# Kernel tuning notes

Hardware: AMD Instinct MI355X
Metric: run time of the kernel (lower is better)

Reference implementation:

```python
import jax, jax.numpy as jnp
import numpy as np
import math

B, CK, CV, O, T, H, W = 2, 64, 512, 2, 16, 30, 54


def setup_inputs() -> dict:
    key = jax.random.key(0)
    k1, k2, k3, k4, k5 = jax.random.split(key, 5)
    return {
        'query_key': jax.random.normal(k1, (B, CK, H, W), jnp.float32),
        'query_selection': jax.random.uniform(k2, (B, CK, H, W), jnp.float32),
        'memory_key': jax.random.normal(k3, (B, CK, T, H, W), jnp.float32),
        'memory_shrinkage': jax.random.uniform(k4, (B, 1, T, H, W), jnp.float32),
        'memory_value': jax.random.normal(k5, (B, O, CV, T, H, W), jnp.float32),
    }


def reference(query_key, query_selection, memory_key, memory_shrinkage, memory_value):
    b, ck, h, w = query_key.shape
    t = memory_key.shape[2]
    n = t * h * w          # memory bank size
    hw = h * w             # query size
    o, cv = memory_value.shape[1], memory_value.shape[2]

    mk = memory_key.reshape(b, ck, n)             # B CK N
    ms = memory_shrinkage.reshape(b, 1, n)        # B 1 N
    qk = query_key.reshape(b, ck, hw)             # B CK HW
    qe = query_selection.reshape(b, ck, hw)       # B CK HW

    # negative squared L2 distance, selection-weighted per channel:
    # -sum_c qe_c * (mk_c - qk_c)^2 = -a_sq + 2ab - b_sq
    a_sq = jnp.einsum('bcn,bcq->bnq', mk * mk, qe)          # B N HW
    two_ab = 2.0 * jnp.einsum('bcn,bcq->bnq', mk, qk * qe)  # B N HW
    b_sq = jnp.sum(qe * qk * qk, axis=1, keepdims=True)     # B 1 HW
    similarity = (-a_sq + two_ab - b_sq)
    # shrinkage scaling + 1/sqrt(CK)
    similarity = similarity * ms.reshape(b, n, 1) * (1.0 / math.sqrt(ck))

    # softmax over the memory axis N
    affinity = jax.nn.softmax(similarity, axis=1)           # B N HW

    # weighted readout
    mv = memory_value.reshape(b, o * cv, n)                 # B (O*CV) N
    mem = jnp.einsum('bvn,bnq->bvq', mv, affinity)          # B (O*CV) HW
    return mem.reshape(b, o, cv, h, w)
```

## Files before the change

kernel.cpp:

```cpp
#include <hip/hip_runtime.h>
#include <stdint.h>

#define CKP 128
#define OCV 1024
#define NTOT 25920
#define HW 1620
#define HWP 1664
#define QT 128
#define VT 256
#define NC 64
#define NQT 13
#define NVT 4
#define CHUNKS_TOTAL 405

typedef _Float16 f16x8 __attribute__((ext_vector_type(8)));
typedef _Float16 f16x4 __attribute__((ext_vector_type(4)));
typedef float f32x4 __attribute__((ext_vector_type(4)));

__device__ __forceinline__ void gload_lds16(const void* g, void* l) {
  __builtin_amdgcn_global_load_lds(
      (const __attribute__((address_space(1))) uint32_t*)g,
      (__attribute__((address_space(3))) uint32_t*)l, 16, 0, 0);
}

__global__ void k_prep_mv(const float* __restrict__ mv, _Float16* __restrict__ mvh) {
  int i = blockIdx.x * 256 + threadIdx.x;
  const float4* s = (const float4*)mv + (size_t)i * 2;
  float4 a = s[0], b = s[1];
  f16x8 o;
  o[0]=(_Float16)a.x; o[1]=(_Float16)a.y; o[2]=(_Float16)a.z; o[3]=(_Float16)a.w;
  o[4]=(_Float16)b.x; o[5]=(_Float16)b.y; o[6]=(_Float16)b.z; o[7]=(_Float16)b.w;
  *((f16x8*)mvh + i) = o;
}

__global__ void k_prep_mk(const float* __restrict__ mk, _Float16* __restrict__ mkp) {
  __shared__ _Float16 LT[64 * CKP];
  int b = blockIdx.y, n0 = blockIdx.x * 64;
  int c4 = threadIdx.x >> 6, nl = threadIdx.x & 63;
  for (int c = c4; c < 64; c += 4) {
    float v = mk[((size_t)(b * 64 + c)) * NTOT + n0 + nl];
    LT[nl * CKP + c]      = (_Float16)v;
    LT[nl * CKP + 64 + c] = (_Float16)(v * v);
  }
  __syncthreads();
  #pragma unroll
  for (int k = 0; k < 4; ++k) {
    int idx = threadIdx.x + 256 * k;
    int n = idx >> 4, c16 = idx & 15;
    *((uint4*)(mkp + ((size_t)b * NTOT + n0 + n) * CKP + c16 * 8)) =
        *((const uint4*)(&LT[n * CKP + c16 * 8]));
  }
}

__global__ void k_prep_q(const float* __restrict__ qk, const float* __restrict__ qe,
                         _Float16* __restrict__ qp, float* __restrict__ bsq) {
  __shared__ _Float16 LT[QT * CKP];
  int b = blockIdx.y, q0 = blockIdx.x * QT;
  int t = threadIdx.x;
  int q = q0 + t;
  bool valid = q < HW;
  float acc = 0.f;
  for (int c = 0; c < 64; ++c) {
    float a = valid ? qk[((size_t)(b * 64 + c)) * HW + q] : 0.f;
    float e = valid ? qe[((size_t)(b * 64 + c)) * HW + q] : 0.f;
    LT[t * CKP + c]      = (_Float16)(2.f * a * e);
    LT[t * CKP + 64 + c] = (_Float16)(-e);
    acc += e * a * a;
  }
  bsq[(size_t)b * HWP + q] = acc;
  __syncthreads();
  #pragma unroll
  for (int k = 0; k < 16; ++k) {
    int idx = t + 128 * k;
    int qq = idx >> 4, c16 = idx & 15;
    *((uint4*)(qp + ((size_t)b * HWP + q0 + qq) * CKP + c16 * 8)) =
        *((const uint4*)(&LT[qq * CKP + c16 * 8]));
  }
}

__launch_bounds__(512, 1)
__global__ void k_main(const _Float16* __restrict__ mvh, const _Float16* __restrict__ mkp,
                       const _Float16* __restrict__ qp, const float* __restrict__ bsq,
                       const float* __restrict__ ms,
                       float* __restrict__ pO, float* __restrict__ lpart,
                       int NS, int CPN) {
  const int qt = blockIdx.x, vt = blockIdx.y;
  const int b = blockIdx.z & 1, nsp = blockIdx.z >> 1;
  const int tid = threadIdx.x;
  const int w = tid >> 6, l = tid & 63;
  const int l15 = l & 15, g = l >> 4;

  __shared__ _Float16 MVs[2][VT * NC];
  __shared__ _Float16 MKs[2][NC * CKP];
  __shared__ _Float16 Ps[2][QT * NC];
  __shared__ float lred[QT * 8];

  const int qw = w & 3, nh = w >> 2;
  const int wv = w & 3, wq = w >> 2;

  const int cBeg = nsp * CPN;
  int ce = cBeg + CPN; if (ce > CHUNKS_TOTAL) ce = CHUNKS_TOTAL;
  const int cEnd = ce;

  const char* mvb[4]; int dmv[4];
  #pragma unroll
  for (int k = 0; k < 4; ++k) {
    int idx = k * 512 + tid;
    int v = idx >> 3, s = idx & 7, j = s ^ (v & 7);
    mvb[k] = (const char*)(mvh + ((size_t)b * OCV + vt * VT + v) * NTOT + j * 8);
    dmv[k] = idx * 16;
  }
  const char* mkb[2]; int dmk[2];
  #pragma unroll
  for (int k = 0; k < 2; ++k) {
    int idx = k * 512 + tid;
    int n = idx >> 4, s = idx & 15, j = s ^ (n & 7);
    mkb[k] = (const char*)(mkp + ((size_t)b * NTOT + n) * CKP + j * 8);
    dmk[k] = idx * 16;
  }
  const float* msb = ms + (size_t)b * NTOT + nh * 32 + g * 4;

  f16x8 qreg[2][4];
  float bq[2];
  #pragma unroll
  for (int j = 0; j < 2; ++j) {
    int q_loc = qw * 32 + j * 16 + l15;
    const _Float16* qrow = qp + ((size_t)b * HWP + qt * QT + q_loc) * CKP;
    #pragma unroll
    for (int ks = 0; ks < 4; ++ks) qreg[j][ks] = *((const f16x8*)(qrow + (ks * 4 + g) * 8));
    bq[j] = bsq[(size_t)b * HWP + qt * QT + q_loc];
  }

  f32x4 acc[4][4];
  #pragma unroll
  for (int i = 0; i < 4; ++i)
    #pragma unroll
    for (int j = 0; j < 4; ++j) acc[i][j] = (f32x4)0.f;
  float lp0 = 0.f, lp1 = 0.f;

  auto stage_mv = [&](int ch, int buf) {
    size_t o = (size_t)ch * (NC * 2);
    char* d = (char*)MVs[buf];
    #pragma unroll
    for (int k = 0; k < 4; ++k) gload_lds16(mvb[k] + o, d + dmv[k]);
  };
  auto stage_mk = [&](int ch, int buf) {
    size_t o = (size_t)ch * (NC * CKP * 2);
    char* d = (char*)MKs[buf];
    #pragma unroll
    for (int k = 0; k < 2; ++k) gload_lds16(mkb[k] + o, d + dmk[k]);
  };

  auto do_S = [&](int kb, int pb, float4 mA, float4 mB) {
    const _Float16* MKc = MKs[kb];
    f32x4 sacc[2][2];
    #pragma unroll
    for (int i2 = 0; i2 < 2; ++i2)
      #pragma unroll
      for (int j = 0; j < 2; ++j) sacc[i2][j] = (f32x4)0.f;
    #pragma unroll
    for (int ks = 0; ks < 4; ++ks) {
      f16x8 af[2];
      #pragma unroll
      for (int i2 = 0; i2 < 2; ++i2) {
        int n_loc = nh * 32 + i2 * 16 + l15;
        af[i2] = *((const f16x8*)(&MKc[n_loc * CKP + (((ks * 4 + g) ^ (n_loc & 7)) * 8)]));
      }
      #pragma unroll
      for (int i2 = 0; i2 < 2; ++i2)
        #pragma unroll
        for (int j = 0; j < 2; ++j)
          sacc[i2][j] = __builtin_amdgcn_mfma_f32_16x16x32_f16(af[i2], qreg[j][ks], sacc[i2][j], 0, 0, 0);
    }
    const float K = 0.125f * 1.44269504f;
    #pragma unroll
    for (int i2 = 0; i2 < 2; ++i2) {
      int nbase = nh * 32 + i2 * 16 + g * 4;
      float m0 = (i2 ? mB.x : mA.x) * K;
      float m1 = (i2 ? mB.y : mA.y) * K;
      float m2 = (i2 ? mB.z : mA.z) * K;
      float m3 = (i2 ? mB.w : mA.w) * K;
      #pragma unroll
      for (int j = 0; j < 2; ++j) {
        int q_loc = qw * 32 + j * 16 + l15;
        float bqv = bq[j];
        float p0 = exp2f((sacc[i2][j][0] - bqv) * m0);
        float p1 = exp2f((sacc[i2][j][1] - bqv) * m1);
        float p2 = exp2f((sacc[i2][j][2] - bqv) * m2);
        float p3 = exp2f((sacc[i2][j][3] - bqv) * m3);
        float psum = (p0 + p1) + (p2 + p3);
        if (j == 0) lp0 += psum; else lp1 += psum;
        f16x4 ph;
        ph[0]=(_Float16)p0; ph[1]=(_Float16)p1; ph[2]=(_Float16)p2; ph[3]=(_Float16)p3;
        int nb = nbase >> 3;
        int off4 = nbase & 7;
        *((f16x4*)(&Ps[pb][q_loc * NC + ((nb ^ (q_loc & 7)) * 8) + off4])) = ph;
      }
    }
  };

  auto do_RO = [&](int mb, int pb) {
    const _Float16* MVc = MVs[mb];
    const _Float16* Pc = Ps[pb];
    #pragma unroll
    for (int ks = 0; ks < 2; ++ks) {
      f16x8 av[4], bp[4];
      #pragma unroll
      for (int i = 0; i < 4; ++i) {
        int v_loc = wv * 64 + i * 16 + l15;
        av[i] = *((const f16x8*)(&MVc[v_loc * NC + (((ks * 4 + g) ^ (v_loc & 7)) * 8)]));
      }
      #pragma unroll
      for (int j = 0; j < 4; ++j) {
        int q_loc = wq * 64 + j * 16 + l15;
        bp[j] = *((const f16x8*)(&Pc[q_loc * NC + (((ks * 4 + g) ^ (q_loc & 7)) * 8)]));
      }
      #pragma unroll
      for (int i = 0; i < 4; ++i)
        #pragma unroll
        for (int j = 0; j < 4; ++j)
          acc[i][j] = __builtin_amdgcn_mfma_f32_16x16x32_f16(av[i], bp[j], acc[i][j], 0, 0, 0);
    }
  };

  stage_mv(cBeg, 0);
  stage_mk(cBeg, 0);
  if (cBeg + 1 < cEnd) stage_mk(cBeg + 1, 1);
  float4 mA0 = *(const float4*)(msb + (size_t)cBeg * NC);
  float4 mB0 = *(const float4*)(msb + (size_t)cBeg * NC + 16);
  asm volatile("s_waitcnt vmcnt(0)" ::: "memory");
  __builtin_amdgcn_s_barrier();
  __builtin_amdgcn_sched_barrier(0);
  do_S(0, 0, mA0, mB0);
  asm volatile("s_waitcnt lgkmcnt(0)" ::: "memory");
  __builtin_amdgcn_s_barrier();
  __builtin_amdgcn_sched_barrier(0);

  const int numCh = cEnd - cBeg;
  for (int i = 0; i < numCh; ++i) {
    const int ch = cBeg + i;
    const int cur = i & 1, nxt = cur ^ 1;
    const bool hv = (ch + 1 < cEnd);
    float4 mA, mB;
    if (hv) {
      mA = *(const float4*)(msb + (size_t)(ch + 1) * NC);
      mB = *(const float4*)(msb + (size_t)(ch + 1) * NC + 16);
    }
    __builtin_amdgcn_sched_barrier(0);
    if (hv) stage_mv(ch + 1, nxt);
    if (ch + 2 < cEnd) stage_mk(ch + 2, cur);
    if (hv) do_S(nxt, nxt, mA, mB);
    do_RO(cur, cur);
    asm volatile("s_waitcnt vmcnt(0) lgkmcnt(0)" ::: "memory");
    __builtin_amdgcn_s_barrier();
    __builtin_amdgcn_sched_barrier(0);
  }

  {
    int q0a = qw * 32 + l15;
    lred[q0a * 8 + nh * 4 + g] = lp0;
    lred[(q0a + 16) * 8 + nh * 4 + g] = lp1;
  }
  __syncthreads();
  if (tid < QT) {
    float s = 0.f;
    #pragma unroll
    for (int j = 0; j < 8; ++j) s += lred[tid * 8 + j];
    lpart[((size_t)(b * NS + nsp)) * HWP + qt * QT + tid] = s;
  }
  #pragma unroll
  for (int i = 0; i < 4; ++i) {
    #pragma unroll
    for (int j = 0; j < 4; ++j) {
      #pragma unroll
      for (int r = 0; r < 4; ++r) {
        int v_glob = vt * VT + wv * 64 + i * 16 + g * 4 + r;
        int q_l = qt * QT + wq * 64 + j * 16 + l15;
        pO[(((size_t)(b * NS + nsp)) * OCV + v_glob) * HWP + q_l] = acc[i][j][r];
      }
    }
  }
}

__global__ void k_reduce(const float* __restrict__ pO, const float* __restrict__ lpart,
                         float* __restrict__ out, int NS) {
  int i = blockIdx.x * 256 + threadIdx.x;
  int q4 = i % 405;
  int rest = i / 405;
  int v = rest & (OCV - 1);
  int b = rest >> 10;
  int q = q4 * 4;
  float apx = 0.f, apy = 0.f, apz = 0.f, apw = 0.f;
  float alx = 0.f, aly = 0.f, alz = 0.f, alw = 0.f;
  for (int s = 0; s < NS; ++s) {
    const float4 p = *((const float4*)(pO + (((size_t)(b * NS + s)) * OCV + v) * HWP + q));
    const float4 lv = *((const float4*)(lpart + ((size_t)(b * NS + s)) * HWP + q));
    apx += p.x; apy += p.y; apz += p.z; apw += p.w;
    alx += lv.x; aly += lv.y; alz += lv.z; alw += lv.w;
  }
  float4 o;
  o.x = apx / alx; o.y = apy / aly; o.z = apz / alz; o.w = apw / alw;
  *((float4*)(out + ((size_t)b * OCV + v) * HW + q)) = o;
}

extern "C" void kernel_launch(void* const* d_in, const int* in_sizes, int n_in,
                              void* d_out, int out_size, void* d_ws, size_t ws_size,
                              hipStream_t stream) {
  const float* qk = (const float*)d_in[0];
  const float* qe = (const float*)d_in[1];
  const float* mk = (const float*)d_in[2];
  const float* ms = (const float*)d_in[3];
  const float* mv = (const float*)d_in[4];
  float* out = (float*)d_out;

  const size_t sz_mvh = (size_t)2 * OCV * NTOT * 2;
  const size_t sz_mkp = (size_t)2 * NTOT * CKP * 2;
  const size_t sz_qp  = (size_t)2 * HWP * CKP * 2;
  const size_t sz_bsq = (size_t)2 * HWP * 4;
  const size_t base   = sz_mvh + sz_mkp + sz_qp + sz_bsq;
  auto need = [&](int ns) {
    return base + (size_t)2 * ns * HWP * 4 + (size_t)2 * ns * OCV * HWP * 4;
  };
  int NS = (ws_size >= need(4)) ? 4 : 2;
  if (ws_size < need(NS)) return;
  const int CPN = (CHUNKS_TOTAL + NS - 1) / NS;

  char* p = (char*)d_ws;
  _Float16* mvh = (_Float16*)p; p += sz_mvh;
  _Float16* mkp = (_Float16*)p; p += sz_mkp;
  _Float16* qp  = (_Float16*)p; p += sz_qp;
  float* bsqw   = (float*)p;    p += sz_bsq;
  float* lpart  = (float*)p;    p += (size_t)2 * NS * HWP * 4;
  float* pO     = (float*)p;

  k_prep_mv<<<25920, 256, 0, stream>>>(mv, mvh);
  k_prep_mk<<<dim3(405, 2), 256, 0, stream>>>(mk, mkp);
  k_prep_q<<<dim3(NQT, 2), QT, 0, stream>>>(qk, qe, qp, bsqw);
  k_main<<<dim3(NQT, NVT, 2 * NS), 512, 0, stream>>>(mvh, mkp, qp, bsqw, ms, pO, lpart, NS, CPN);
  k_reduce<<<3240, 256, 0, stream>>>(pO, lpart, out, NS);
}
```

Before: 580.1 us.

## Fix split-N to two and remap workgroups to XCDs for L2 reuse

Hardcodes a two-way split of the memory axis and launches a flat 1-D grid of 208 workgroups. Workgroup ids are decoded so that all blocks on the same XCD share a batch, N-split and pair of value tiles, so their mk/mv streams can be reused within that XCD's L2. It also halves the partial outputs the reduction kernel reads and unrolls its split loop. In exchange, fewer workgroups than CUs are launched, which leaves some CUs idle, and the split count no longer adapts to the workspace size.

Result: faster. 561.3 us (-3.2%).

```diff
diff --git a/kernel.cpp b/kernel.cpp
--- a/kernel.cpp
+++ b/kernel.cpp
@@ -10,8 +10,9 @@
 #define VT 256
 #define NC 64
 #define NQT 13
-#define NVT 4
+#define NS 2
 #define CHUNKS_TOTAL 405
+#define CHUNK_SPLIT 203
 
 typedef _Float16 f16x8 __attribute__((ext_vector_type(8)));
 typedef _Float16 f16x4 __attribute__((ext_vector_type(4)));
@@ -82,10 +83,15 @@
 __global__ void k_main(const _Float16* __restrict__ mvh, const _Float16* __restrict__ mkp,
                        const _Float16* __restrict__ qp, const float* __restrict__ bsq,
                        const float* __restrict__ ms,
-                       float* __restrict__ pO, float* __restrict__ lpart,
-                       int NS, int CPN) {
-  const int qt = blockIdx.x, vt = blockIdx.y;
-  const int b = blockIdx.z & 1, nsp = blockIdx.z >> 1;
+                       float* __restrict__ pO, float* __restrict__ lpart) {
+  const int wgid = blockIdx.x;
+  const int xcd = wgid & 7, kk = wgid >> 3;
+  const int gsel = (kk >= NQT) ? 1 : 0;
+  const int qt = kk - gsel * NQT;
+  const int vt = ((xcd & 1) << 1) | gsel;
+  const int bn = xcd >> 1;
+  const int b = bn >> 1, nsp = bn & 1;
+
   const int tid = threadIdx.x;
   const int w = tid >> 6, l = tid & 63;
   const int l15 = l & 15, g = l >> 4;
@@ -98,9 +104,8 @@
   const int qw = w & 3, nh = w >> 2;
   const int wv = w & 3, wq = w >> 2;
 
-  const int cBeg = nsp * CPN;
-  int ce = cBeg + CPN; if (ce > CHUNKS_TOTAL) ce = CHUNKS_TOTAL;
-  const int cEnd = ce;
+  const int cBeg = nsp ? CHUNK_SPLIT : 0;
+  const int cEnd = nsp ? CHUNKS_TOTAL : CHUNK_SPLIT;
 
   const char* mvb[4]; int dmv[4];
   #pragma unroll
@@ -283,7 +288,7 @@
 }
 
 __global__ void k_reduce(const float* __restrict__ pO, const float* __restrict__ lpart,
-                         float* __restrict__ out, int NS) {
+                         float* __restrict__ out) {
   int i = blockIdx.x * 256 + threadIdx.x;
   int q4 = i % 405;
   int rest = i / 405;
@@ -292,6 +297,7 @@
   int q = q4 * 4;
   float apx = 0.f, apy = 0.f, apz = 0.f, apw = 0.f;
   float alx = 0.f, aly = 0.f, alz = 0.f, alw = 0.f;
+  #pragma unroll
   for (int s = 0; s < NS; ++s) {
     const float4 p = *((const float4*)(pO + (((size_t)(b * NS + s)) * OCV + v) * HWP + q));
     const float4 lv = *((const float4*)(lpart + ((size_t)(b * NS + s)) * HWP + q));
@@ -317,13 +323,9 @@
   const size_t sz_mkp = (size_t)2 * NTOT * CKP * 2;
   const size_t sz_qp  = (size_t)2 * HWP * CKP * 2;
   const size_t sz_bsq = (size_t)2 * HWP * 4;
-  const size_t base   = sz_mvh + sz_mkp + sz_qp + sz_bsq;
-  auto need = [&](int ns) {
-    return base + (size_t)2 * ns * HWP * 4 + (size_t)2 * ns * OCV * HWP * 4;
-  };
-  int NS = (ws_size >= need(4)) ? 4 : 2;
-  if (ws_size < need(NS)) return;
-  const int CPN = (CHUNKS_TOTAL + NS - 1) / NS;
+  const size_t need = sz_mvh + sz_mkp + sz_qp + sz_bsq
+                    + (size_t)2 * NS * HWP * 4 + (size_t)2 * NS * OCV * HWP * 4;
+  if (ws_size < need) return;
 
   char* p = (char*)d_ws;
   _Float16* mvh = (_Float16*)p; p += sz_mvh;
@@ -336,6 +338,6 @@
   k_prep_mv<<<25920, 256, 0, stream>>>(mv, mvh);
   k_prep_mk<<<dim3(405, 2), 256, 0, stream>>>(mk, mkp);
   k_prep_q<<<dim3(NQT, 2), QT, 0, stream>>>(qk, qe, qp, bsqw);
-  k_main<<<dim3(NQT, NVT, 2 * NS), 512, 0, stream>>>(mvh, mkp, qp, bsqw, ms, pO, lpart, NS, CPN);
-  k_reduce<<<3240, 256, 0, stream>>>(pO, lpart, out, NS);
-}
+  k_main<<<8 * 26, 512, 0, stream>>>(mvh, mkp, qp, bsqw, ms, pO, lpart);
+  k_reduce<<<3240, 256, 0, stream>>>(pO, lpart, out);
+}
```
